# Kernel tuning notes

Measured on AMD Instinct MI355X. Metric: run time of the kernel, lower is better.

The kernel has to match this reference:

```python
import jax, jax.numpy as jnp
import numpy as np

IN_SIZE = 256
N_THETA = 180
GRID = int(np.ceil(np.sqrt(2.0) * IN_SIZE))  # 363, == detector size == it_size


def _ramp_filter(P):
    # f is the spatial-domain ramp filter impulse response (Ram-Lak)
    n = np.concatenate([np.arange(1, P / 2 + 1, 2), np.arange(P / 2 - 1, 0, -2)])
    f = np.zeros(P, np.float32)
    f[0] = 0.25
    f[1::2] = -1.0 / (np.pi * n) ** 2
    # torch code multiplies both re/im by the real part of fft(f): complex * real scalar
    return jnp.asarray(2.0 * np.real(np.fft.fft(f)), jnp.float32)  # [P]


def _apply_ramp(x):
    # x: [N,C,S,A]; FFT filter along detector axis (2) with zero padding
    S = x.shape[2]
    P = max(64, int(2 ** np.ceil(np.log2(2 * S))))
    xp = jnp.pad(x, ((0, 0), (0, 0), (0, P - S), (0, 0)))
    filt = _ramp_filter(P)  # [P]
    spec = jnp.fft.fft(xp, axis=2) * filt[:, None]
    return jnp.real(jnp.fft.ifft(spec, axis=2))[:, :, :S, :].astype(x.dtype)


def _polar_T(G):
    # T[a,i,j] = xgrid*cos(theta_a) - ygrid*sin(theta_a), grids via meshgrid(ij)
    unit = jnp.linspace(-1.0, 1.0, G, dtype=jnp.float32)
    yg, xg = jnp.meshgrid(unit, unit, indexing='ij')
    th = jnp.deg2rad(jnp.arange(N_THETA, dtype=jnp.float32))  # [A]
    return xg[None] * jnp.cos(th)[:, None, None] - yg[None] * jnp.sin(th)[:, None, None]  # [A,G,G]


def _backproject(sino, T):
    # sino: [N,C,S,A]; grid X coord = i*2/(A-1)-1 picks column a exactly
    # (align_corners=True), so bilinear reduces to 1D lerp along the detector.
    N, C, S, A = sino.shape
    G = T.shape[1]
    pos = (T + 1.0) * (S - 1) / 2.0  # [A,G,G] fractional detector index
    i0 = jnp.floor(pos)
    w = (pos - i0).reshape(A, -1)  # [A,G*G]
    i0i = i0.astype(jnp.int32)
    i1i = i0i + 1
    ok0 = ((i0i >= 0) & (i0i < S)).reshape(A, -1)  # zeros padding outside
    ok1 = ((i1i >= 0) & (i1i < S)).reshape(A, -1)
    i0c = jnp.clip(i0i, 0, S - 1).reshape(A, -1)
    i1c = jnp.clip(i1i, 0, S - 1).reshape(A, -1)
    st = jnp.moveaxis(sino, 3, 2)  # [N,C,A,S]
    v0 = jnp.take_along_axis(st, i0c[None, None], axis=3)  # [N,C,A,G*G]
    v1 = jnp.take_along_axis(st, i1c[None, None], axis=3)
    w0 = jnp.where(ok0, 1.0 - w, 0.0)[None, None]
    w1 = jnp.where(ok1, w, 0.0)[None, None]
    reco = (v0 * w0 + v1 * w1).sum(axis=2)  # sum over angles
    return reco.reshape(N, C, G, G)


def setup_inputs() -> dict:
    key = jax.random.key(0)
    x = jax.random.normal(key, (4, 1, GRID, N_THETA), dtype=jnp.float32)
    return {"x": x}


def reference(x) -> jnp.ndarray:
    # filtered backprojection (inverse Radon), circle=False
    x = _apply_ramp(x)
    T = _polar_T(GRID)
    reco = _backproject(x, T)  # [N,C,G,G]
    # crop back to in_size x in_size (negative padding in torch code)
    W, G = IN_SIZE, GRID
    pad = G - W
    pad_before = (W + pad) // 2 - W // 2
    reco = reco[:, :, pad_before:G - (pad - pad_before), pad_before:G - (pad - pad_before)]
    return reco * (jnp.pi / (2.0 * N_THETA))
```

## Files before the change

kernel.cpp:

```cpp
#include <hip/hip_runtime.h>

#define S_DIM 363
#define S_P   368
#define A_DIM 180
#define OUT_W 256
#define F_PI 3.14159265358979323846f
#define W_C  (-2.0f / (F_PI * F_PI))

typedef float    f4 __attribute__((ext_vector_type(4)));
typedef _Float16 h4 __attribute__((ext_vector_type(4)));
union HU { uint2 u; h4 h; };

__device__ uint2  g_sino[A_DIM * S_P];
__device__ float2 g_csn[A_DIM];

__global__ __launch_bounds__(256) void iradon_filter_kernel(
        const float* __restrict__ x) {
    __shared__ f4 xs4[S_DIM];

    const int a   = blockIdx.x;
    const int tid = threadIdx.x;

    {
        f4 v;
        v.x = x[(0 * S_DIM + tid) * A_DIM + a];
        v.y = x[(1 * S_DIM + tid) * A_DIM + a];
        v.z = x[(2 * S_DIM + tid) * A_DIM + a];
        v.w = x[(3 * S_DIM + tid) * A_DIM + a];
        xs4[tid] = v;
        const int s2 = tid + 256;
        if (s2 < S_DIM) {
            f4 w;
            w.x = x[(0 * S_DIM + s2) * A_DIM + a];
            w.y = x[(1 * S_DIM + s2) * A_DIM + a];
            w.z = x[(2 * S_DIM + s2) * A_DIM + a];
            w.w = x[(3 * S_DIM + s2) * A_DIM + a];
            xs4[s2] = w;
        }
    }
    if (tid == 254) {
        float th = (float)a * (F_PI / 180.0f);
        g_csn[a] = make_float2(cosf(th), sinf(th));
    }
    __syncthreads();

    {
        const int t1 = tid;
        const int t2 = tid + 256;
        f4 acc1 = 0.5f * xs4[t1];
        f4 acc2 = 0.5f * xs4[(t2 < S_DIM) ? t2 : 0];

        const float tf1 = (float)t1;
        const float tf2 = (float)t2;
        const int   s0  = 1 - (tid & 1);
        float sf = (float)s0;
        #pragma unroll 4
        for (int s = s0; s < S_DIM; s += 2, sf += 2.0f) {
            f4 v = xs4[s];
            float d1 = sf - tf1;
            float d2 = sf - tf2;
            float w1 = W_C * __builtin_amdgcn_rcpf(d1 * d1);
            float w2 = W_C * __builtin_amdgcn_rcpf(d2 * d2);
            acc1 += w1 * v;
            acc2 += w2 * v;
        }

        HU r1; r1.h = __builtin_convertvector(acc1, h4);
        g_sino[a * S_P + 1 + t1] = r1.u;
        if (t2 < S_DIM) {
            HU r2; r2.h = __builtin_convertvector(acc2, h4);
            g_sino[a * S_P + 1 + t2] = r2.u;
        }
    }
    if (tid == 252) { HU z; z.u.x = 0u; z.u.y = 0u; g_sino[a * S_P + 0]   = z.u; }
    if (tid == 253) { HU z; z.u.x = 0u; z.u.y = 0u; g_sino[a * S_P + 364] = z.u; }
}

__global__ __launch_bounds__(256) void iradon_backproject_kernel(
        float* __restrict__ out) {
    __shared__ float2 csn[A_DIM];
    __shared__ f4 red[256];

    const int tid = threadIdx.x;
    if (tid < A_DIM) csn[tid] = g_csn[tid];
    __syncthreads();

    const int px = tid & 63;
    const int q  = tid >> 6;
    const int j  = blockIdx.x * 64 + px;
    const int i  = blockIdx.y;

    const float jj  = (float)(j - 128);
    const float nii = (float)(128 - i);

    f4 acc = (f4)0.0f;
    const int a0 = q * 45;
    #pragma unroll 5
    for (int m = 0; m < 45; ++m) {
        const int a = a0 + m;
        const float2 cn = csn[a];
        float pos = fmaf(jj, cn.x, fmaf(nii, cn.y, 181.0f));
        float f   = floorf(pos);
        int   k1  = (int)f + 1;
        float w1  = pos - f;
        float w0  = 1.0f - w1;
        const uint2* __restrict__ row = g_sino + a * S_P;
        HU lo, hi;
        lo.u = row[k1];
        hi.u = row[k1 + 1];
        acc.x = fmaf((float)lo.h.x, w0, fmaf((float)hi.h.x, w1, acc.x));
        acc.y = fmaf((float)lo.h.y, w0, fmaf((float)hi.h.y, w1, acc.y));
        acc.z = fmaf((float)lo.h.z, w0, fmaf((float)hi.h.z, w1, acc.z));
        acc.w = fmaf((float)lo.h.w, w0, fmaf((float)hi.h.w, w1, acc.w));
    }

    red[tid] = acc;
    __syncthreads();

    if (tid < 64) {
        f4 r = red[tid] + red[tid + 64] + red[tid + 128] + red[tid + 192];
        r *= (F_PI / 360.0f);
        const int jo   = blockIdx.x * 64 + tid;
        const size_t p = (size_t)blockIdx.y * OUT_W + jo;
        out[p]              = r.x;
        out[p +     65536]  = r.y;
        out[p + 2 * 65536]  = r.z;
        out[p + 3 * 65536]  = r.w;
    }
}

extern "C" void kernel_launch(void* const* d_in, const int* in_sizes, int n_in,
                              void* d_out, int out_size, void* d_ws, size_t ws_size,
                              hipStream_t stream) {
    const float* x = (const float*)d_in[0];
    float* out = (float*)d_out;

    iradon_filter_kernel<<<dim3(A_DIM), 256, 0, stream>>>(x);
    iradon_backproject_kernel<<<dim3(4, OUT_W), 256, 0, stream>>>(out);
}
```

Before: 71.71 us.

## Split filter convolution across 768 threads with two-way partial-sum reduction

The filter kernel now launches 768 threads per angle block instead of 256. Each output tap's convolution is split into two stride-4 partial sums computed by different threads, and the halves are combined through a shared-memory reduction. Input loading is spread over all threads with scalar stores into the interleaved shared layout. The aim is to shorten the serial per-thread loop of the filter stage, at the cost of an extra barrier, more shared memory and a larger block, while the grid is still only 180 blocks.

```diff
diff --git a/kernel.cpp b/kernel.cpp
--- a/kernel.cpp
+++ b/kernel.cpp
@@ -14,66 +14,55 @@
 __device__ uint2  g_sino[A_DIM * S_P];
 __device__ float2 g_csn[A_DIM];
 
-__global__ __launch_bounds__(256) void iradon_filter_kernel(
+__global__ __launch_bounds__(768) void iradon_filter_kernel(
         const float* __restrict__ x) {
     __shared__ f4 xs4[S_DIM];
+    __shared__ f4 red[726];
 
     const int a   = blockIdx.x;
     const int tid = threadIdx.x;
 
     {
-        f4 v;
-        v.x = x[(0 * S_DIM + tid) * A_DIM + a];
-        v.y = x[(1 * S_DIM + tid) * A_DIM + a];
-        v.z = x[(2 * S_DIM + tid) * A_DIM + a];
-        v.w = x[(3 * S_DIM + tid) * A_DIM + a];
-        xs4[tid] = v;
-        const int s2 = tid + 256;
-        if (s2 < S_DIM) {
-            f4 w;
-            w.x = x[(0 * S_DIM + s2) * A_DIM + a];
-            w.y = x[(1 * S_DIM + s2) * A_DIM + a];
-            w.z = x[(2 * S_DIM + s2) * A_DIM + a];
-            w.w = x[(3 * S_DIM + s2) * A_DIM + a];
-            xs4[s2] = w;
+        float* lds = (float*)xs4;
+        int n = tid;
+        #pragma unroll 2
+        for (int r = 0; r < 2; ++r, n += 768) {
+            if (n < 4 * S_DIM) {
+                int b = (n >= 3 * S_DIM) ? 3 : (n >= 2 * S_DIM) ? 2
+                      : (n >= S_DIM) ? 1 : 0;
+                int s = n - b * S_DIM;
+                lds[s * 4 + b] = x[n * A_DIM + a];
+            }
         }
     }
-    if (tid == 254) {
+    if (tid == 728) {
         float th = (float)a * (F_PI / 180.0f);
         g_csn[a] = make_float2(cosf(th), sinf(th));
     }
     __syncthreads();
 
-    {
-        const int t1 = tid;
-        const int t2 = tid + 256;
-        f4 acc1 = 0.5f * xs4[t1];
-        f4 acc2 = 0.5f * xs4[(t2 < S_DIM) ? t2 : 0];
+    if (tid < 726) {
+        const int t  = (tid >= S_DIM) ? tid - S_DIM : tid;
+        const int p0 = (tid >= S_DIM) ? ((t + 3) & 3) : ((t + 1) & 3);
+        f4 acc = (f4)0.0f;
+        float df = (float)(p0 - t);
+        #pragma unroll 4
+        for (int s = p0; s < S_DIM; s += 4, df += 4.0f) {
+            f4 v = xs4[s];
+            float w = W_C * __builtin_amdgcn_rcpf(df * df);
+            acc += w * v;
+        }
+        red[tid] = acc;
+    }
+    __syncthreads();
 
-        const float tf1 = (float)t1;
-        const float tf2 = (float)t2;
-        const int   s0  = 1 - (tid & 1);
-        float sf = (float)s0;
-        #pragma unroll 4
-        for (int s = s0; s < S_DIM; s += 2, sf += 2.0f) {
-            f4 v = xs4[s];
-            float d1 = sf - tf1;
-            float d2 = sf - tf2;
-            float w1 = W_C * __builtin_amdgcn_rcpf(d1 * d1);
-            float w2 = W_C * __builtin_amdgcn_rcpf(d2 * d2);
-            acc1 += w1 * v;
-            acc2 += w2 * v;
-        }
-
-        HU r1; r1.h = __builtin_convertvector(acc1, h4);
-        g_sino[a * S_P + 1 + t1] = r1.u;
-        if (t2 < S_DIM) {
-            HU r2; r2.h = __builtin_convertvector(acc2, h4);
-            g_sino[a * S_P + 1 + t2] = r2.u;
-        }
+    if (tid < S_DIM) {
+        f4 tot = 0.5f * xs4[tid] + red[tid] + red[tid + S_DIM];
+        HU r; r.h = __builtin_convertvector(tot, h4);
+        g_sino[a * S_P + 1 + tid] = r.u;
     }
-    if (tid == 252) { HU z; z.u.x = 0u; z.u.y = 0u; g_sino[a * S_P + 0]   = z.u; }
-    if (tid == 253) { HU z; z.u.x = 0u; z.u.y = 0u; g_sino[a * S_P + 364] = z.u; }
+    if (tid == 726) { HU z; z.u.x = 0u; z.u.y = 0u; g_sino[a * S_P + 0]   = z.u; }
+    if (tid == 727) { HU z; z.u.x = 0u; z.u.y = 0u; g_sino[a * S_P + 364] = z.u; }
 }
 
 __global__ __launch_bounds__(256) void iradon_backproject_kernel(
@@ -135,6 +124,6 @@
     const float* x = (const float*)d_in[0];
     float* out = (float*)d_out;
 
-    iradon_filter_kernel<<<dim3(A_DIM), 256, 0, stream>>>(x);
+    iradon_filter_kernel<<<dim3(A_DIM), 768, 0, stream>>>(x);
     iradon_backproject_kernel<<<dim3(4, OUT_W), 256, 0, stream>>>(out);
 }
```

Result: faster. 68.71 us (-4.2%).
